# Kernel tuning notes

Hardware: AMD Instinct MI355X
Metric: run time of the kernel (lower is better)

## Reference

```python
import jax, jax.numpy as jnp
import numpy as np
import math

JOINT_DIM = 16
D_MODEL = 128
NUM_HEADS = 8
HEAD_DIM = D_MODEL // NUM_HEADS


def kinematic_adjacency():
    adj = np.zeros((JOINT_DIM, JOINT_DIM), dtype=np.float32)
    skeleton = [(0, 1), (1, 2), (2, 3), (0, 4), (4, 5), (5, 6), (0, 7), (7, 8),
                (8, 9), (0, 10), (10, 11), (11, 12), (0, 13), (13, 14), (14, 15)]
    for p, c in skeleton:
        adj[p, c] = 1.0
        adj[c, p] = 1.0
    sym = [(4, 7), (5, 8), (6, 9), (10, 13), (11, 14), (12, 15)]
    for a, b in sym:
        adj[a, b] += 0.8
        adj[b, a] += 0.8
    adj += np.eye(JOINT_DIM, dtype=np.float32)
    return jnp.asarray(adj)


def setup_inputs() -> dict:
    key = jax.random.key(0)
    ks = jax.random.split(key, 9)
    B, S = 64, 512
    s3 = 1.0 / math.sqrt(3.0)
    sd = 1.0 / math.sqrt(D_MODEL)
    return {
        "x": jax.random.normal(ks[0], (B, S, JOINT_DIM, 3), dtype=jnp.float32),
        "Wq": jax.random.uniform(ks[1], (3, D_MODEL), jnp.float32, -s3, s3),
        "bq": jax.random.uniform(ks[2], (D_MODEL,), jnp.float32, -s3, s3),
        "Wk": jax.random.uniform(ks[3], (3, D_MODEL), jnp.float32, -s3, s3),
        "bk": jax.random.uniform(ks[4], (D_MODEL,), jnp.float32, -s3, s3),
        "Wv": jax.random.uniform(ks[5], (3, D_MODEL), jnp.float32, -s3, s3),
        "bv": jax.random.uniform(ks[6], (D_MODEL,), jnp.float32, -s3, s3),
        "Wo": jax.random.uniform(ks[7], (D_MODEL, D_MODEL), jnp.float32, -sd, sd),
        "bo": jax.random.uniform(ks[8], (D_MODEL,), jnp.float32, -sd, sd),
    }


def reference(x, Wq, bq, Wk, bk, Wv, bv, Wo, bo):
    B, S, J, _ = x.shape
    adj = kinematic_adjacency()  # [J, J]

    def split_heads(t):  # [B,S,J,D] -> [B,S,H,J,hd]
        return t.reshape(B, S, J, NUM_HEADS, HEAD_DIM).transpose(0, 1, 3, 2, 4)

    q = split_heads(x @ Wq + bq)
    k = split_heads(x @ Wk + bk)
    v = split_heads(x @ Wv + bv)

    # scores get adjacency bias BEFORE the 1/sqrt(head_dim) scaling (as in source)
    scores = jnp.einsum('bshjd,bshkd->bshjk', q, k)
    scores = (scores + adj) / math.sqrt(HEAD_DIM)
    w = jax.nn.softmax(scores, axis=-1)  # dropout inactive (eval)
    ctx = jnp.einsum('bshjk,bshkd->bshjd', w, v)
    ctx = ctx.transpose(0, 1, 3, 2, 4).reshape(B, S, J, D_MODEL)
    return ctx @ Wo + bo  # [B,S,J,D]
```

## Files before the change

kernel.cpp:

```cpp
#include <hip/hip_runtime.h>

#define NJ   16
#define DM   128
#define NH   8
#define P    8
#define NPASS 4

typedef __attribute__((ext_vector_type(8))) short bf16x8;
typedef __attribute__((ext_vector_type(4))) float f32x4;

__constant__ __align__(16) float c_adj[NJ * NJ] = {
    1,1,0,0, 1,0,0,1, 0,0,1,0, 0,1,0,0,
    1,1,1,0, 0,0,0,0, 0,0,0,0, 0,0,0,0,
    0,1,1,1, 0,0,0,0, 0,0,0,0, 0,0,0,0,
    0,0,1,1, 0,0,0,0, 0,0,0,0, 0,0,0,0,
    1,0,0,0, 1,1,0,0.8f, 0,0,0,0, 0,0,0,0,
    0,0,0,0, 1,1,1,0, 0.8f,0,0,0, 0,0,0,0,
    0,0,0,0, 0,1,1,0, 0,0.8f,0,0, 0,0,0,0,
    1,0,0,0, 0.8f,0,0,1, 1,0,0,0, 0,0,0,0,
    0,0,0,0, 0,0.8f,0,1, 1,1,0,0, 0,0,0,0,
    0,0,0,0, 0,0,0.8f,0, 1,1,0,0, 0,0,0,0,
    1,0,0,0, 0,0,0,0, 0,0,1,1, 0,0.8f,0,0,
    0,0,0,0, 0,0,0,0, 0,0,1,1, 1,0,0.8f,0,
    0,0,0,0, 0,0,0,0, 0,0,0,1, 1,0,0,0.8f,
    1,0,0,0, 0,0,0,0, 0,0,0.8f,0, 0,1,1,0,
    0,0,0,0, 0,0,0,0, 0,0,0,0.8f, 0,1,1,1,
    0,0,0,0, 0,0,0,0, 0,0,0,0, 0.8f,0,1,1
};

#define WS_BP_W   0
#define WS_PACK_W 128
#define WS_GF_W   256

__device__ __forceinline__ unsigned short f2bf(float f) {
    union { float f; unsigned u; } v; v.f = f;
    unsigned u = v.u;
    u += 0x7FFFu + ((u >> 16) & 1u);
    return (unsigned short)(u >> 16);
}
__device__ __forceinline__ unsigned pack2bf(float lo, float hi) {
    return (unsigned)f2bf(lo) | ((unsigned)f2bf(hi) << 16);
}

__global__ __launch_bounds__(256) void skel_setup_kernel(
    const float* __restrict__ Wq, const float* __restrict__ bq,
    const float* __restrict__ Wk, const float* __restrict__ bk,
    const float* __restrict__ Wv, const float* __restrict__ bv,
    const float* __restrict__ Wo, const float* __restrict__ bo,
    unsigned* __restrict__ wsu)
{
    const int b = blockIdx.x, t = threadIdx.x;
    float* wsf = (float*)wsu;

    if (b < 8) {
        const int idx = b * 256 + t;
        const int ctl = idx >> 2, i = idx & 3;
        const int ct = ctl >> 6, l = ctl & 63;
        const int n  = ct * 16 + (l & 15);
        const int kb = (l >> 4) * 8;
        float v[2];
#pragma unroll
        for (int s = 0; s < 2; ++s) {
            const int k = kb + 2 * i + s;
            const int h = k >> 2, r = k & 3;
            float acc = 0.f;
            if (r < 3) {
#pragma unroll
                for (int dh = 0; dh < 16; ++dh)
                    acc += Wv[r * DM + h * 16 + dh] * Wo[(h * 16 + dh) * DM + n];
            }
            v[s] = acc;
        }
        wsu[WS_GF_W + idx] = pack2bf(v[0], v[1]);
        return;
    }
    if (t < 128) {
        const int n = t;
        float bv_ = bo[n];
        for (int d = 0; d < DM; ++d) bv_ += bv[d] * Wo[d * DM + n];
        wsf[WS_BP_W + n] = bv_;
    } else if (t < 128 + NH) {
        const int h = t - 128;
        float* o = &wsf[WS_PACK_W + h * 16];
#pragma unroll
        for (int r = 0; r < 3; ++r)
#pragma unroll
            for (int c = 0; c < 3; ++c) {
                float acc = 0.f;
#pragma unroll
                for (int dh = 0; dh < 16; ++dh)
                    acc += Wq[r * DM + h * 16 + dh] * Wk[c * DM + h * 16 + dh];
                o[r * 3 + c] = acc;
            }
#pragma unroll
        for (int r = 0; r < 3; ++r) {
            float aa = 0.f, cc = 0.f;
#pragma unroll
            for (int dh = 0; dh < 16; ++dh) {
                aa += Wq[r * DM + h * 16 + dh] * bk[h * 16 + dh];
                cc += Wk[r * DM + h * 16 + dh] * bq[h * 16 + dh];
            }
            o[9 + r]  = aa;
            o[12 + r] = cc;
        }
        float dd = 0.f;
#pragma unroll
        for (int dh = 0; dh < 16; ++dh) dd += bq[h * 16 + dh] * bk[h * 16 + dh];
        o[15] = dd;
    }
}

__global__ __launch_bounds__(256) void skel_main_kernel(
    const float* __restrict__ x,
    const unsigned* __restrict__ wsu,
    float* __restrict__ out,
    int npos)
{
    const int t = threadIdx.x;
    const long pos0 = (long)blockIdx.x * P;
    const float* wsf = (const float*)wsu;

    __shared__ float sx[P][48];
    __shared__ float sc[128];
    __shared__ __align__(16) float st[2][NH][17][4];
    __shared__ __align__(16) unsigned sxb[P * NJ][16];
    __shared__ __align__(16) unsigned sgf[2048];
    __shared__ float sbp[128];

    for (int i = t; i < P * 48; i += 256) {
        const long gi = pos0 * 48 + i;
        sx[i / 48][i % 48] = (gi < (long)npos * 48) ? x[gi] : 0.f;
    }
    if (t < 128) {
        sbp[t] = wsf[WS_BP_W + t];
        sc[t]  = wsf[WS_PACK_W + t];
    }
    {
        const uint4* gsrc = (const uint4*)&wsu[WS_GF_W];
        uint4* gdst = (uint4*)sgf;
        gdst[t]       = gsrc[t];
        gdst[t + 256] = gsrc[t + 256];
    }
    __syncthreads();

    const int p2  = t >> 7;
    const int rem = t & 127;
    const int h   = rem >> 4;
    const int kj  = rem & 15;
    const float* Mh = &sc[h * 16];

    for (int pass = 0; pass < NPASS; ++pass) {
        const int p = pass * 2 + p2;
        const float x0 = sx[p][kj * 3 + 0];
        const float x1 = sx[p][kj * 3 + 1];
        const float x2 = sx[p][kj * 3 + 2];

        st[p2][h][kj][0] = Mh[0] * x0 + Mh[1] * x1 + Mh[2] * x2;
        st[p2][h][kj][1] = Mh[3] * x0 + Mh[4] * x1 + Mh[5] * x2;
        st[p2][h][kj][2] = Mh[6] * x0 + Mh[7] * x1 + Mh[8] * x2;
        st[p2][h][kj][3] = Mh[12] * x0 + Mh[13] * x1 + Mh[14] * x2 + Mh[15];
        __syncthreads();

        {
            const int j = kj;
            const float u = Mh[9] * x0 + Mh[10] * x1 + Mh[11] * x2;

            const float4* adjq = (const float4*)&c_adj[j * NJ];
            const float4 a0 = adjq[0], a1 = adjq[1], a2 = adjq[2], a3 = adjq[3];
            float adjr[NJ] = { a0.x,a0.y,a0.z,a0.w, a1.x,a1.y,a1.z,a1.w,
                               a2.x,a2.y,a2.z,a2.w, a3.x,a3.y,a3.z,a3.w };

            float s[NJ];
            float mx = -1e30f;
#pragma unroll
            for (int k = 0; k < NJ; ++k) {
                const float4 tk = *(const float4*)&st[p2][h][k][0];
                float sv = x0 * tk.x + x1 * tk.y + x2 * tk.z + tk.w + u;
                sv = (sv + adjr[k]) * 0.25f;
                s[k] = sv;
                mx = fmaxf(mx, sv);
            }
            float sum = 0.f;
#pragma unroll
            for (int k = 0; k < NJ; ++k) {
                const float e = __expf(s[k] - mx);
                s[k] = e;
                sum += e;
            }
            const float inv = 1.f / sum;

            float xb0 = 0.f, xb1 = 0.f, xb2 = 0.f;
#pragma unroll
            for (int k = 0; k < NJ; ++k) {
                const float wk = s[k] * inv;
                xb0 += wk * sx[p][k * 3 + 0];
                xb1 += wk * sx[p][k * 3 + 1];
                xb2 += wk * sx[p][k * 3 + 2];
            }
            const int row = p * NJ + j;
            sxb[row][2 * h + 0] = pack2bf(xb0, xb1);
            sxb[row][2 * h + 1] = pack2bf(xb2, 0.f);
        }
        __syncthreads();
    }

    {
        const int wv = t >> 6, l = t & 63;
        const int lrow = l & 15, lk = l >> 4;

        float bpv[8];
#pragma unroll
        for (int ct = 0; ct < 8; ++ct) bpv[ct] = sbp[ct * 16 + lrow];

#pragma unroll
        for (int ri = 0; ri < 2; ++ri) {
            const int rt = wv * 2 + ri;
            if (pos0 + rt >= npos) continue;
            const bf16x8 a = *(const bf16x8*)&sxb[rt * 16 + lrow][lk * 4];
            float* obase = out + (pos0 + rt) * (long)(NJ * DM);
#pragma unroll
            for (int ct = 0; ct < 8; ++ct) {
                const bf16x8 bfr = *(const bf16x8*)&sgf[(ct * 64 + l) * 4];
                f32x4 acc = { bpv[ct], bpv[ct], bpv[ct], bpv[ct] };
                acc = __builtin_amdgcn_mfma_f32_16x16x32_bf16(a, bfr, acc, 0, 0, 0);
                const int col = ct * 16 + lrow;
#pragma unroll
                for (int r = 0; r < 4; ++r) {
                    const int jrow = lk * 4 + r;
                    obase[jrow * DM + col] = acc[r];
                }
            }
        }
    }
}

extern "C" void kernel_launch(void* const* d_in, const int* in_sizes, int n_in,
                              void* d_out, int out_size, void* d_ws, size_t ws_size,
                              hipStream_t stream) {
    const float* x  = (const float*)d_in[0];
    const float* Wq = (const float*)d_in[1];
    const float* bq = (const float*)d_in[2];
    const float* Wk = (const float*)d_in[3];
    const float* bk = (const float*)d_in[4];
    const float* Wv = (const float*)d_in[5];
    const float* bv = (const float*)d_in[6];
    const float* Wo = (const float*)d_in[7];
    const float* bo = (const float*)d_in[8];
    float* out    = (float*)d_out;
    unsigned* wsu = (unsigned*)d_ws;

    const int npos = in_sizes[0] / (NJ * 3);
    skel_setup_kernel<<<9, 256, 0, stream>>>(Wq, bq, Wk, bk, Wv, bv, Wo, bo, wsu);
    const int grid = (npos + P - 1) / P;
    skel_main_kernel<<<grid, 256, 0, stream>>>(x, wsu, out, npos);
}
```

Measured before the change: 74.72 us.

## Interleave MFMA output projection into each attention pass and drop softmax max

```diff
diff --git a/kernel.cpp b/kernel.cpp
--- a/kernel.cpp
+++ b/kernel.cpp
@@ -120,7 +120,7 @@
     const long pos0 = (long)blockIdx.x * P;
     const float* wsf = (const float*)wsu;
 
-    __shared__ float sx[P][48];
+    __shared__ __align__(16) float sx[P][48];
     __shared__ float sc[128];
     __shared__ __align__(16) float st[2][NH][17][4];
     __shared__ __align__(16) unsigned sxb[P * NJ][16];
@@ -149,6 +149,18 @@
     const int kj  = rem & 15;
     const float* Mh = &sc[h * 16];
 
+    const int wv = t >> 6, l = t & 63;
+    const int lrow = l & 15, lk = l >> 4;
+    const int pi = wv >> 1;
+    const int cb = (wv & 1) * 4;
+    bf16x8 bfr[4];
+    float  bpv[4];
+#pragma unroll
+    for (int cti = 0; cti < 4; ++cti) {
+        bfr[cti] = *(const bf16x8*)&sgf[((cb + cti) * 64 + l) * 4];
+        bpv[cti] = sbp[(cb + cti) * 16 + lrow];
+    }
+
     for (int pass = 0; pass < NPASS; ++pass) {
         const int p = pass * 2 + p2;
         const float x0 = sx[p][kj * 3 + 0];
@@ -171,63 +183,55 @@
                                a2.x,a2.y,a2.z,a2.w, a3.x,a3.y,a3.z,a3.w };
 
             float s[NJ];
-            float mx = -1e30f;
+            float sum = 0.f;
 #pragma unroll
             for (int k = 0; k < NJ; ++k) {
                 const float4 tk = *(const float4*)&st[p2][h][k][0];
                 float sv = x0 * tk.x + x1 * tk.y + x2 * tk.z + tk.w + u;
                 sv = (sv + adjr[k]) * 0.25f;
-                s[k] = sv;
-                mx = fmaxf(mx, sv);
-            }
-            float sum = 0.f;
-#pragma unroll
-            for (int k = 0; k < NJ; ++k) {
-                const float e = __expf(s[k] - mx);
+                const float e = __expf(sv);
                 s[k] = e;
                 sum += e;
             }
             const float inv = 1.f / sum;
 
+            float xr[48];
+            {
+                const float4* sxq = (const float4*)&sx[p][0];
+#pragma unroll
+                for (int q = 0; q < 12; ++q) *(float4*)&xr[q * 4] = sxq[q];
+            }
             float xb0 = 0.f, xb1 = 0.f, xb2 = 0.f;
 #pragma unroll
             for (int k = 0; k < NJ; ++k) {
-                const float wk = s[k] * inv;
-                xb0 += wk * sx[p][k * 3 + 0];
-                xb1 += wk * sx[p][k * 3 + 1];
-                xb2 += wk * sx[p][k * 3 + 2];
-            }
-            const int row = p * NJ + j;
+                const float e = s[k];
+                xb0 += e * xr[k * 3 + 0];
+                xb1 += e * xr[k * 3 + 1];
+                xb2 += e * xr[k * 3 + 2];
+            }
+            xb0 *= inv; xb1 *= inv; xb2 *= inv;
+
+            const int row = p * NJ + kj;
             sxb[row][2 * h + 0] = pack2bf(xb0, xb1);
             sxb[row][2 * h + 1] = pack2bf(xb2, 0.f);
         }
         __syncthreads();
-    }
-
-    {
-        const int wv = t >> 6, l = t & 63;
-        const int lrow = l & 15, lk = l >> 4;
-
-        float bpv[8];
-#pragma unroll
-        for (int ct = 0; ct < 8; ++ct) bpv[ct] = sbp[ct * 16 + lrow];
-
-#pragma unroll
-        for (int ri = 0; ri < 2; ++ri) {
-            const int rt = wv * 2 + ri;
-            if (pos0 + rt >= npos) continue;
-            const bf16x8 a = *(const bf16x8*)&sxb[rt * 16 + lrow][lk * 4];
-            float* obase = out + (pos0 + rt) * (long)(NJ * DM);
-#pragma unroll
-            for (int ct = 0; ct < 8; ++ct) {
-                const bf16x8 bfr = *(const bf16x8*)&sgf[(ct * 64 + l) * 4];
-                f32x4 acc = { bpv[ct], bpv[ct], bpv[ct], bpv[ct] };
-                acc = __builtin_amdgcn_mfma_f32_16x16x32_bf16(a, bfr, acc, 0, 0, 0);
-                const int col = ct * 16 + lrow;
-#pragma unroll
-                for (int r = 0; r < 4; ++r) {
-                    const int jrow = lk * 4 + r;
-                    obase[jrow * DM + col] = acc[r];
+
+        {
+            const int p_out = pass * 2 + pi;
+            if (pos0 + p_out < npos) {
+                const bf16x8 a = *(const bf16x8*)&sxb[p_out * NJ + lrow][lk * 4];
+                float* obase = out + (pos0 + p_out) * (long)(NJ * DM);
+#pragma unroll
+                for (int cti = 0; cti < 4; ++cti) {
+                    f32x4 acc = { bpv[cti], bpv[cti], bpv[cti], bpv[cti] };
+                    acc = __builtin_amdgcn_mfma_f32_16x16x32_bf16(a, bfr[cti], acc, 0, 0, 0);
+                    const int col = (cb + cti) * 16 + lrow;
+#pragma unroll
+                    for (int r = 0; r < 4; ++r) {
+                        const int jrow = lk * 4 + r;
+                        obase[jrow * DM + col] = acc[r];
+                    }
                 }
             }
         }
```

Measured after the change: 78.40 us. 4.9% more time.

## Restructure attention into per-wave work with exp2 softmax and vectorized transposed MFMA stores

Applied to the files above, without the earlier changes.

```diff
diff --git a/kernel.cpp b/kernel.cpp
--- a/kernel.cpp
+++ b/kernel.cpp
@@ -4,12 +4,12 @@
 #define DM   128
 #define NH   8
 #define P    8
-#define NPASS 4
+#define CL   0.36067376022224085f
 
 typedef __attribute__((ext_vector_type(8))) short bf16x8;
 typedef __attribute__((ext_vector_type(4))) float f32x4;
 
-__constant__ __align__(16) float c_adj[NJ * NJ] = {
+__constant__ float c_adj[NJ * NJ] = {
     1,1,0,0, 1,0,0,1, 0,0,1,0, 0,1,0,0,
     1,1,1,0, 0,0,0,0, 0,0,0,0, 0,0,0,0,
     0,1,1,1, 0,0,0,0, 0,0,0,0, 0,0,0,0,
@@ -90,7 +90,7 @@
 #pragma unroll
                 for (int dh = 0; dh < 16; ++dh)
                     acc += Wq[r * DM + h * 16 + dh] * Wk[c * DM + h * 16 + dh];
-                o[r * 3 + c] = acc;
+                o[r * 3 + c] = acc * CL;
             }
 #pragma unroll
         for (int r = 0; r < 3; ++r) {
@@ -100,13 +100,13 @@
                 aa += Wq[r * DM + h * 16 + dh] * bk[h * 16 + dh];
                 cc += Wk[r * DM + h * 16 + dh] * bq[h * 16 + dh];
             }
-            o[9 + r]  = aa;
-            o[12 + r] = cc;
+            o[9 + r]  = aa * CL;
+            o[12 + r] = cc * CL;
         }
         float dd = 0.f;
 #pragma unroll
         for (int dh = 0; dh < 16; ++dh) dd += bq[h * 16 + dh] * bk[h * 16 + dh];
-        o[15] = dd;
+        o[15] = dd * CL;
     }
 }
 
@@ -120,20 +120,26 @@
     const long pos0 = (long)blockIdx.x * P;
     const float* wsf = (const float*)wsu;
 
-    __shared__ float sx[P][48];
-    __shared__ float sc[128];
-    __shared__ __align__(16) float st[2][NH][17][4];
-    __shared__ __align__(16) unsigned sxb[P * NJ][16];
+    __shared__ __align__(16) float    sx4[P][NJ][4];
+    __shared__ float                  sc[128];
+    __shared__ __align__(16) float    st[4][NH][17][4];
+    __shared__ __align__(16) unsigned sxb[4][NJ * 16];
     __shared__ __align__(16) unsigned sgf[2048];
-    __shared__ float sbp[128];
-
-    for (int i = t; i < P * 48; i += 256) {
-        const long gi = pos0 * 48 + i;
-        sx[i / 48][i % 48] = (gi < (long)npos * 48) ? x[gi] : 0.f;
-    }
+    __shared__ __align__(16) float    sbp[128];
+
     if (t < 128) {
-        sbp[t] = wsf[WS_BP_W + t];
-        sc[t]  = wsf[WS_PACK_W + t];
+        const int p = t >> 4, j = t & 15;
+        const long pidx = pos0 + p;
+        const long base = pidx * 48 + j * 3;
+        const bool ok = pidx < npos;
+        sx4[p][j][0] = ok ? x[base + 0] : 0.f;
+        sx4[p][j][1] = ok ? x[base + 1] : 0.f;
+        sx4[p][j][2] = ok ? x[base + 2] : 0.f;
+        sx4[p][j][3] = 0.f;
+    } else {
+        const int i = t - 128;
+        sc[i]  = wsf[WS_PACK_W + i];
+        sbp[i] = wsf[WS_BP_W + i];
     }
     {
         const uint4* gsrc = (const uint4*)&wsu[WS_GF_W];
@@ -143,92 +149,80 @@
     }
     __syncthreads();
 
-    const int p2  = t >> 7;
-    const int rem = t & 127;
-    const int h   = rem >> 4;
-    const int kj  = rem & 15;
-    const float* Mh = &sc[h * 16];
-
-    for (int pass = 0; pass < NPASS; ++pass) {
-        const int p = pass * 2 + p2;
-        const float x0 = sx[p][kj * 3 + 0];
-        const float x1 = sx[p][kj * 3 + 1];
-        const float x2 = sx[p][kj * 3 + 2];
-
-        st[p2][h][kj][0] = Mh[0] * x0 + Mh[1] * x1 + Mh[2] * x2;
-        st[p2][h][kj][1] = Mh[3] * x0 + Mh[4] * x1 + Mh[5] * x2;
-        st[p2][h][kj][2] = Mh[6] * x0 + Mh[7] * x1 + Mh[8] * x2;
-        st[p2][h][kj][3] = Mh[12] * x0 + Mh[13] * x1 + Mh[14] * x2 + Mh[15];
-        __syncthreads();
-
+    const int wv = t >> 6, l = t & 63;
+    const int h  = l >> 3, j0 = l & 7;
+
+    float m[16];
+#pragma unroll
+    for (int i = 0; i < 16; ++i) m[i] = sc[h * 16 + i];
+    float adj0[NJ], adj1[NJ];
+#pragma unroll
+    for (int k = 0; k < NJ; ++k) {
+        adj0[k] = c_adj[j0 * NJ + k] * CL;
+        adj1[k] = c_adj[(j0 + 8) * NJ + k] * CL;
+    }
+
+    const int jB = l & 15, lkB = l >> 4;
+
+    for (int it = 0; it < 2; ++it) {
+        const int p = wv * 2 + it;
+
+        const f32x4 xa = *(const f32x4*)&sx4[p][j0];
+        const f32x4 xb = *(const f32x4*)&sx4[p][j0 + 8];
         {
-            const int j = kj;
-            const float u = Mh[9] * x0 + Mh[10] * x1 + Mh[11] * x2;
-
-            const float4* adjq = (const float4*)&c_adj[j * NJ];
-            const float4 a0 = adjq[0], a1 = adjq[1], a2 = adjq[2], a3 = adjq[3];
-            float adjr[NJ] = { a0.x,a0.y,a0.z,a0.w, a1.x,a1.y,a1.z,a1.w,
-                               a2.x,a2.y,a2.z,a2.w, a3.x,a3.y,a3.z,a3.w };
-
-            float s[NJ];
-            float mx = -1e30f;
-#pragma unroll
-            for (int k = 0; k < NJ; ++k) {
-                const float4 tk = *(const float4*)&st[p2][h][k][0];
-                float sv = x0 * tk.x + x1 * tk.y + x2 * tk.z + tk.w + u;
-                sv = (sv + adjr[k]) * 0.25f;
-                s[k] = sv;
-                mx = fmaxf(mx, sv);
-            }
-            float sum = 0.f;
-#pragma unroll
-            for (int k = 0; k < NJ; ++k) {
-                const float e = __expf(s[k] - mx);
-                s[k] = e;
-                sum += e;
-            }
-            const float inv = 1.f / sum;
-
-            float xb0 = 0.f, xb1 = 0.f, xb2 = 0.f;
-#pragma unroll
-            for (int k = 0; k < NJ; ++k) {
-                const float wk = s[k] * inv;
-                xb0 += wk * sx[p][k * 3 + 0];
-                xb1 += wk * sx[p][k * 3 + 1];
-                xb2 += wk * sx[p][k * 3 + 2];
-            }
-            const int row = p * NJ + j;
-            sxb[row][2 * h + 0] = pack2bf(xb0, xb1);
-            sxb[row][2 * h + 1] = pack2bf(xb2, 0.f);
-        }
-        __syncthreads();
-    }
-
-    {
-        const int wv = t >> 6, l = t & 63;
-        const int lrow = l & 15, lk = l >> 4;
-
-        float bpv[8];
-#pragma unroll
-        for (int ct = 0; ct < 8; ++ct) bpv[ct] = sbp[ct * 16 + lrow];
-
-#pragma unroll
-        for (int ri = 0; ri < 2; ++ri) {
-            const int rt = wv * 2 + ri;
-            if (pos0 + rt >= npos) continue;
-            const bf16x8 a = *(const bf16x8*)&sxb[rt * 16 + lrow][lk * 4];
-            float* obase = out + (pos0 + rt) * (long)(NJ * DM);
+            f32x4 tv;
+            tv.x = m[0]*xa.x + m[1]*xa.y + m[2]*xa.z;
+            tv.y = m[3]*xa.x + m[4]*xa.y + m[5]*xa.z;
+            tv.z = m[6]*xa.x + m[7]*xa.y + m[8]*xa.z;
+            tv.w = m[12]*xa.x + m[13]*xa.y + m[14]*xa.z + m[15];
+            *(f32x4*)&st[wv][h][j0][0] = tv;
+            tv.x = m[0]*xb.x + m[1]*xb.y + m[2]*xb.z;
+            tv.y = m[3]*xb.x + m[4]*xb.y + m[5]*xb.z;
+            tv.z = m[6]*xb.x + m[7]*xb.y + m[8]*xb.z;
+            tv.w = m[12]*xb.x + m[13]*xb.y + m[14]*xb.z + m[15];
+            *(f32x4*)&st[wv][h][j0 + 8][0] = tv;
+        }
+
+        const float u0 = m[9]*xa.x + m[10]*xa.y + m[11]*xa.z;
+        const float u1 = m[9]*xb.x + m[10]*xb.y + m[11]*xb.z;
+        float sum0 = 0.f, sum1 = 0.f;
+        float a00 = 0.f, a01 = 0.f, a02 = 0.f;
+        float a10 = 0.f, a11 = 0.f, a12 = 0.f;
+#pragma unroll
+        for (int k = 0; k < NJ; ++k) {
+            const f32x4 tk = *(const f32x4*)&st[wv][h][k][0];
+            const f32x4 xk = *(const f32x4*)&sx4[p][k];
+            const float s0 = xa.x*tk.x + xa.y*tk.y + xa.z*tk.z + (tk.w + u0 + adj0[k]);
+            const float s1 = xb.x*tk.x + xb.y*tk.y + xb.z*tk.z + (tk.w + u1 + adj1[k]);
+            const float e0 = exp2f(s0);
+            const float e1 = exp2f(s1);
+            sum0 += e0; sum1 += e1;
+            a00 += e0 * xk.x; a01 += e0 * xk.y; a02 += e0 * xk.z;
+            a10 += e1 * xk.x; a11 += e1 * xk.y; a12 += e1 * xk.z;
+        }
+        const float inv0 = __builtin_amdgcn_rcpf(sum0);
+        const float inv1 = __builtin_amdgcn_rcpf(sum1);
+
+        {
+            uint2 w0, w1;
+            w0.x = pack2bf(a00 * inv0, a01 * inv0);
+            w0.y = pack2bf(a02 * inv0, 0.f);
+            w1.x = pack2bf(a10 * inv1, a11 * inv1);
+            w1.y = pack2bf(a12 * inv1, 0.f);
+            *(uint2*)&sxb[wv][j0 * 16 + 2 * h]       = w0;
+            *(uint2*)&sxb[wv][(j0 + 8) * 16 + 2 * h] = w1;
+        }
+
+        if (pos0 + p < npos) {
+            const bf16x8 bvec = *(const bf16x8*)&sxb[wv][jB * 16 + lkB * 4];
+            float* obase = out + (pos0 + p) * (long)(NJ * DM) + jB * DM + lkB * 4;
 #pragma unroll
             for (int ct = 0; ct < 8; ++ct) {
-                const bf16x8 bfr = *(const bf16x8*)&sgf[(ct * 64 + l) * 4];
-                f32x4 acc = { bpv[ct], bpv[ct], bpv[ct], bpv[ct] };
-                acc = __builtin_amdgcn_mfma_f32_16x16x32_bf16(a, bfr, acc, 0, 0, 0);
-                const int col = ct * 16 + lrow;
-#pragma unroll
-                for (int r = 0; r < 4; ++r) {
-                    const int jrow = lk * 4 + r;
-                    obase[jrow * DM + col] = acc[r];
-                }
+                const bf16x8 ga = *(const bf16x8*)&sgf[(ct * 64 + l) * 4];
+                const f32x4 bp4 = *(const f32x4*)&sbp[ct * 16 + lkB * 4];
+                f32x4 acc = bp4;
+                acc = __builtin_amdgcn_mfma_f32_16x16x32_bf16(ga, bvec, acc, 0, 0, 0);
+                *(f32x4*)(obase + ct * 16) = acc;
             }
         }
     }
```

Result: slower. 78.66 us (+5.3%).
